# Optimization experiments

Measured on AMD Instinct MI355X. Metric: run time of the kernel, lower is better.

Reference implementation:

```python
import jax, jax.numpy as jnp
import numpy as np

LAYER_NUM = 2
NUM_CLS = 128
HIDDEN = 256
NUM_NODES = 1024


def setup_inputs() -> dict:
    key = jax.random.key(0)
    ks = jax.random.split(key, 12)
    s = 0.05
    return {
        "x": jax.random.normal(ks[0], (NUM_NODES, HIDDEN), jnp.float32),
        "knowledge": jax.random.uniform(ks[1], (NUM_CLS, NUM_CLS), jnp.float32) / NUM_CLS,
        "w3w": jax.random.normal(ks[2], (HIDDEN, 2 * HIDDEN), jnp.float32) * s,
        "b3w": jax.random.normal(ks[3], (HIDDEN,), jnp.float32) * s,
        "u3": jax.random.normal(ks[4], (HIDDEN, HIDDEN), jnp.float32) * s,
        "bu3": jax.random.normal(ks[5], (HIDDEN,), jnp.float32) * s,
        "w4w": jax.random.normal(ks[6], (HIDDEN, 2 * HIDDEN), jnp.float32) * s,
        "b4w": jax.random.normal(ks[7], (HIDDEN,), jnp.float32) * s,
        "w5w": jax.random.normal(ks[8], (HIDDEN, 2 * HIDDEN), jnp.float32) * s,
        "b5w": jax.random.normal(ks[9], (HIDDEN,), jnp.float32) * s,
        "u5": jax.random.normal(ks[10], (HIDDEN, HIDDEN), jnp.float32) * s,
        "bu5": jax.random.normal(ks[11], (HIDDEN,), jnp.float32) * s,
    }


def reference(x, knowledge, w3w, b3w, u3, bu3, w4w, b4w, w5w, b5w, u5, bu5):
    N, H = x.shape
    C = knowledge.shape[0]
    # hidden[n, c, :] = x[n, :]  (repeat per class)
    hidden = jnp.broadcast_to(x[:, None, :], (N, C, H))
    for _ in range(LAYER_NUM):
        hs = hidden.sum(0)                      # [C, H]
        diff = hs[None, :, :] - hidden          # [N, C, H]
        # knowledge.T @ diff_n  and  knowledge @ diff_n, vectorized over nodes
        left = jnp.einsum('kc,nkh->nch', knowledge, diff)
        right = jnp.einsum('ck,nkh->nch', knowledge, diff)
        av = jnp.concatenate([left, right], axis=-1).reshape(N * C, 2 * H)
        h = hidden.reshape(N * C, H)
        uh3 = h @ u3.T + bu3                    # shared: rv uses fc_eq3_u (source quirk)
        zv = jax.nn.sigmoid(av @ w3w.T + b3w + uh3)
        rv = jax.nn.sigmoid(av @ w4w.T + b4w + uh3)
        hv = jnp.tanh(av @ w5w.T + b5w + (rv * h) @ u5.T + bu5)
        h = (1.0 - zv) * h + zv * hv
        hidden = h.reshape(N, C, H)
    return hidden
```

## Files before the change

### kernel.cpp

```cpp
#include <hip/hip_runtime.h>
#include <cstdint>
#include <cstddef>


#define NODES 1024
#define NCLS  128
#define HID   256

using frag  = __attribute__((ext_vector_type(8))) short;
using frag4 = __attribute__((ext_vector_type(4))) short;
using f32x4 = __attribute__((ext_vector_type(4))) float;

__device__ __forceinline__ float bf2f(unsigned short h){
  unsigned int u = ((unsigned int)h) << 16;
  float f; __builtin_memcpy(&f, &u, 4); return f;
}
__device__ __forceinline__ unsigned short f2bf(float f){
  unsigned int u; __builtin_memcpy(&u, &f, 4);
  u = (u + 0x7fffu + ((u >> 16) & 1u)) >> 16;
  return (unsigned short)u;
}
__device__ __forceinline__ float sigm(float x){ return 1.0f/(1.0f + __expf(-x)); }
__device__ __forceinline__ float tanh_fast(float x){ return 1.0f - 2.0f/(__expf(2.0f*x) + 1.0f); }

#define GLOBAL_AS(p) ((const __attribute__((address_space(1))) void*)(p))
#define LDS_AS(p)    ((__attribute__((address_space(3))) void*)(p))
#define MFMA16 __builtin_amdgcn_mfma_f32_16x16x32_bf16

template<int OUT_BF16>
__global__ __launch_bounds__(256) void gemm_bf16(
    const unsigned short* __restrict__ A0, int ldA0, int K0,
    const unsigned short* __restrict__ A1, int ldA1,
    const unsigned short* __restrict__ BT, int ldB, long bStride,
    void* __restrict__ Cptr, int ldC,
    int Ntiles, int Ktot, unsigned int aMask, int Mtiles)
{
  __shared__ unsigned short As[4096];
  __shared__ unsigned short Bs[4096];
  const int t   = threadIdx.x;
  const int bid = blockIdx.x;
  const int xcd = bid & 7, slot = bid >> 3;
  const int mtPerX = (Mtiles >= 8) ? (Mtiles >> 3) : 1;
  const int mt = xcd * mtPerX + slot / Ntiles;
  const int nt = slot % Ntiles;
  const int lane = t & 63, w = t >> 6;
  const int wm = w >> 1, wn = w & 1;
  const int r = lane & 15, q = lane >> 4;
  const int m0 = mt * 128, n0 = nt * 128;
  const unsigned short* Bbase = BT + (size_t)mt * (size_t)bStride;

  f32x4 acc[4][4] = {};

  for (int kb = 0; kb < Ktot; kb += 32) {
#pragma unroll
    for (int i = 0; i < 2; ++i) {
      int u  = i * 256 + t;
      int mi = u >> 2;
      int kc = (u & 3) * 8;
      int k  = kb + kc;
      const unsigned short* ga;
      if (k < K0) ga = A0 + (size_t)((unsigned int)(m0 + mi) & aMask) * (size_t)ldA0 + k;
      else        ga = A1 + (size_t)(m0 + mi) * (size_t)ldA1 + (k - K0);
      __builtin_amdgcn_global_load_lds(GLOBAL_AS(ga), LDS_AS(&As[u * 8]), 16, 0, 0);
      const unsigned short* gb = Bbase + (size_t)(n0 + mi) * (size_t)ldB + k;
      __builtin_amdgcn_global_load_lds(GLOBAL_AS(gb), LDS_AS(&Bs[u * 8]), 16, 0, 0);
    }
    __syncthreads();

    frag af[4], bf_[4];
#pragma unroll
    for (int x = 0; x < 4; ++x) {
      af[x]  = *(const frag*)&As[(wm * 64 + x * 16 + r) * 32 + q * 8];
      bf_[x] = *(const frag*)&Bs[(wn * 64 + x * 16 + r) * 32 + q * 8];
    }
#pragma unroll
    for (int x = 0; x < 4; ++x)
#pragma unroll
      for (int y = 0; y < 4; ++y)
        acc[x][y] = MFMA16(af[x], bf_[y], acc[x][y], 0, 0, 0);
    __syncthreads();
  }

#pragma unroll
  for (int x = 0; x < 4; ++x) {
#pragma unroll
    for (int y = 0; y < 4; ++y) {
      int col = n0 + wn * 64 + y * 16 + r;
#pragma unroll
      for (int g = 0; g < 4; ++g) {
        long row = m0 + wm * 64 + x * 16 + q * 4 + g;
        if (OUT_BF16) ((unsigned short*)Cptr)[row * (long)ldC + col] = f2bf(acc[x][y][g]);
        else          ((float*)Cptr)[row * (long)ldC + col] = acc[x][y][g];
      }
    }
  }
}

__global__ __launch_bounds__(512, 2) void gemm_pre(
    const unsigned short* __restrict__ AVH, const unsigned short* __restrict__ H1,
    const unsigned short* __restrict__ WB, unsigned short* __restrict__ PRE)
{
  __shared__ __align__(16) unsigned short SM[65536];
  const int t   = threadIdx.x;
  const int bid = blockIdx.x;
  const int xcd = bid & 7, slot = bid >> 3;
  const int mt = xcd * 64 + slot / 3;
  const int ct = slot % 3;
  const int lane = t & 63, w = t >> 6;
  const int wm = w >> 2, wn = w & 3;
  const int r = lane & 15, q = lane >> 4;
  const int m0 = mt * 256;
  const unsigned short* Wrow = WB + (size_t)(ct * 256) * 768;
  const int nkt = (ct < 2) ? 12 : 8;

  unsigned short* const Ab0 = SM;
  unsigned short* const Ab1 = SM + 16384;
  unsigned short* const Bb0 = SM + 32768;
  unsigned short* const Bb1 = SM + 49152;

  f32x4 acc[8][4] = {};

  const int smi = t >> 3, sc = t & 7;

  auto ISSUE_A = [&](unsigned short* dst, int kt, int rbase) {
    int row = rbase + smi;
    int gc = sc ^ (row & 7);
    const unsigned short* ga;
    if (kt < 8) ga = AVH + (size_t)(m0 + row) * 512 + kt * 64 + gc * 8;
    else        ga = H1  + (size_t)(m0 + row) * 256 + (kt - 8) * 64 + gc * 8;
    __builtin_amdgcn_global_load_lds(GLOBAL_AS(ga), LDS_AS(&dst[row * 64 + sc * 8]), 16, 0, 0);
  };
  auto ISSUE_B = [&](unsigned short* dst, int kt, int rbase) {
    int row = rbase + smi;
    int gc = sc ^ (row & 7);
    __builtin_amdgcn_global_load_lds(GLOBAL_AS(Wrow + (size_t)row * 768 + kt * 64 + gc * 8),
                                     LDS_AS(&dst[row * 64 + sc * 8]), 16, 0, 0);
  };

  ISSUE_B(Bb0, 0, 0); ISSUE_B(Bb0, 0, 64); ISSUE_B(Bb0, 0, 128); ISSUE_B(Bb0, 0, 192);
  ISSUE_A(Ab0, 0, 0); ISSUE_A(Ab0, 0, 128); ISSUE_A(Ab0, 0, 64); ISSUE_A(Ab0, 0, 192);
  asm volatile("s_waitcnt vmcnt(2)" ::: "memory");
  __builtin_amdgcn_s_barrier();

#define PRE_PHASE(XG0, ISSUES, TAIL)                                         \
    {                                                                        \
      int ra0 = wm * 128 + (XG0) * 16 + r, ra1 = ra0 + 16;                   \
      frag a00 = *(const frag*)&A[ra0 * 64 + ((q ^ (ra0 & 7)) * 8)];         \
      frag a01 = *(const frag*)&A[ra0 * 64 + (((4 + q) ^ (ra0 & 7)) * 8)];   \
      frag a10 = *(const frag*)&A[ra1 * 64 + ((q ^ (ra1 & 7)) * 8)];         \
      frag a11 = *(const frag*)&A[ra1 * 64 + (((4 + q) ^ (ra1 & 7)) * 8)];   \
      ISSUES;                                                                \
      __builtin_amdgcn_s_setprio(1);                                         \
      _Pragma("unroll")                                                      \
      for (int y = 0; y < 4; ++y) {                                          \
        acc[(XG0)][y]     = MFMA16(a00, bf[y][0], acc[(XG0)][y], 0, 0, 0);   \
        acc[(XG0)][y]     = MFMA16(a01, bf[y][1], acc[(XG0)][y], 0, 0, 0);   \
        acc[(XG0)+1][y]   = MFMA16(a10, bf[y][0], acc[(XG0)+1][y], 0, 0, 0); \
        acc[(XG0)+1][y]   = MFMA16(a11, bf[y][1], acc[(XG0)+1][y], 0, 0, 0); \
      }                                                                      \
      __builtin_amdgcn_s_setprio(0);                                         \
      TAIL;                                                                  \
      asm volatile("" ::: "memory");                                         \
      __builtin_amdgcn_s_barrier();                                          \
    }

  for (int kt = 0; kt < nkt; ++kt) {
    unsigned short* A  = (kt & 1) ? Ab1 : Ab0;
    unsigned short* B  = (kt & 1) ? Bb1 : Bb0;
    unsigned short* An = (kt & 1) ? Ab0 : Ab1;
    unsigned short* Bn = (kt & 1) ? Bb0 : Bb1;
    const bool more = (kt + 1 < nkt);

    frag bf[4][2];
#pragma unroll
    for (int y = 0; y < 4; ++y) {
      int rb = wn * 64 + y * 16 + r;
      bf[y][0] = *(const frag*)&B[rb * 64 + ((q ^ (rb & 7)) * 8)];
      bf[y][1] = *(const frag*)&B[rb * 64 + (((4 + q) ^ (rb & 7)) * 8)];
    }

    PRE_PHASE(0,
      { if (more) { ISSUE_B(Bn, kt + 1, 0); ISSUE_B(Bn, kt + 1, 64); } },
      { })
    PRE_PHASE(2,
      { if (more) { ISSUE_B(Bn, kt + 1, 128); ISSUE_B(Bn, kt + 1, 192); } },
      { if (more) asm volatile("s_waitcnt vmcnt(4)" ::: "memory");
        else      asm volatile("s_waitcnt vmcnt(0)" ::: "memory"); })
    PRE_PHASE(4,
      { if (more) { ISSUE_A(An, kt + 1, 0); ISSUE_A(An, kt + 1, 128); } },
      { })
    PRE_PHASE(6,
      { if (more) { ISSUE_A(An, kt + 1, 64); ISSUE_A(An, kt + 1, 192); } },
      { if (more) asm volatile("s_waitcnt vmcnt(2)" ::: "memory"); })
  }
#undef PRE_PHASE

  unsigned short* L = SM;
#pragma unroll
  for (int xg = 0; xg < 8; ++xg) {
#pragma unroll
    for (int y = 0; y < 4; ++y) {
      int j = wn * 64 + y * 16 + r;
      int jc = j >> 3, jl = j & 7;
#pragma unroll
      for (int g = 0; g < 4; ++g) {
        int c = wm * 128 + xg * 16 + q * 4 + g;
        L[c * 256 + ((jc ^ (c & 31)) * 8) + jl] = f2bf(acc[xg][y][g]);
      }
    }
  }
  __syncthreads();
#pragma unroll
  for (int rr = 0; rr < 16; ++rr) {
    int unit = rr * 512 + t;
    int row = unit >> 5, ch = unit & 31;
    frag v = *(const frag*)&L[row * 256 + ((ch ^ (row & 31)) * 8)];
    *(frag*)&PRE[(size_t)(m0 + row) * 768 + ct * 256 + ch * 8] = v;
  }
}

__global__ __launch_bounds__(256, 2) void gemm_l1(
    const float* __restrict__ XW, const float* __restrict__ SW,
    const float* __restrict__ x,
    const float* __restrict__ b3, const float* __restrict__ b4,
    const float* __restrict__ b5, const float* __restrict__ bu3,
    const float* __restrict__ bu5,
    const float* __restrict__ colsum, const float* __restrict__ rowsum,
    const unsigned short* __restrict__ u5b,
    const unsigned short* __restrict__ KTbN, const unsigned short* __restrict__ KbN,
    unsigned short* __restrict__ H1, unsigned short* __restrict__ AVH)
{
  __shared__ unsigned short SM[17408];
  unsigned short* As = SM;
  unsigned short* Bs = SM + 4096;
  unsigned short* L  = SM;
  __shared__ float tP1[256], tP2[256], tP3[256], tX[256];
  __shared__ float tZ1[256], tZ2[256], tZ3[256];
  __shared__ float tV1[256], tV2[256], tV3[256];
  __shared__ float tCS[128], tRS[128];

  const int t = threadIdx.x, bid = blockIdx.x;
  const int xcd = bid & 7, slot = bid >> 3;
  const int n  = xcd * 128 + (slot >> 1);
  const int nt = slot & 1;
  const int lane = t & 63, w = t >> 6, wm = w >> 1, wn = w & 1;
  const int r = lane & 15, q = lane >> 4;
  const int n0 = nt * 128;
  const float* xw = XW + (size_t)n * 1792;

  {
    int i = t;
    float xwi0 = xw[i], xwi1 = xw[256 + i], xwi2 = xw[512 + i], xwi3 = xw[768 + i];
    float xwi4 = xw[1024 + i], xwi5 = xw[1280 + i], xwu = xw[1536 + i];
    tP1[i] = SW[512 + i] - xwi2;
    tP2[i] = SW[768 + i] - xwi3;
    tP3[i] = xwu + b4[i] + bu3[i];
    tX[i]  = x[(size_t)n * HID + i];
    tZ1[i] = SW[i] - xwi0;
    tZ2[i] = SW[256 + i] - xwi1;
    tZ3[i] = xwu + b3[i] + bu3[i];
    tV1[i] = SW[1024 + i] - xwi4;
    tV2[i] = SW[1280 + i] - xwi5;
    tV3[i] = b5[i] + bu5[i];
    if (t < 128) { tCS[t] = colsum[t]; tRS[t] = rowsum[t]; }
  }
  __syncthreads();

  f32x4 acc[4][4] = {};

  for (int kb = 0; kb < 256; kb += 32) {
#pragma unroll
    for (int i = 0; i < 2; ++i) {
      int u  = i * 256 + t;
      int mi = u >> 2;
      int c  = u & 3;
      int k  = kb + c * 8;
      int gc = c ^ ((mi >> 1) & 3);
      __builtin_amdgcn_global_load_lds(GLOBAL_AS(u5b + (size_t)(n0 + mi) * 256 + kb + gc * 8),
                                       LDS_AS(&Bs[u * 8]), 16, 0, 0);
      float cs = tCS[mi], rs = tRS[mi];
      frag a;
#pragma unroll
      for (int e = 0; e < 8; ++e) {
        int i2 = k + e;
        float pre = cs * tP1[i2] + rs * tP2[i2] + tP3[i2];
        a[e] = (short)f2bf(sigm(pre) * tX[i2]);
      }
      *(frag*)&As[mi * 32 + (gc * 8)] = a;
    }
    __syncthreads();

    frag af[4], bf_[4];
#pragma unroll
    for (int xx = 0; xx < 4; ++xx) {
      int ra = wm * 64 + xx * 16 + r;
      int rb = wn * 64 + xx * 16 + r;
      af[xx]  = *(const frag*)&As[ra * 32 + ((q ^ ((ra >> 1) & 3)) * 8)];
      bf_[xx] = *(const frag*)&Bs[rb * 32 + ((q ^ ((rb >> 1) & 3)) * 8)];
    }
#pragma unroll
    for (int xx = 0; xx < 4; ++xx)
#pragma unroll
      for (int y = 0; y < 4; ++y)
        acc[xx][y] = MFMA16(af[xx], bf_[y], acc[xx][y], 0, 0, 0);
    __syncthreads();
  }

#pragma unroll
  for (int xx = 0; xx < 4; ++xx) {
#pragma unroll
    for (int y = 0; y < 4; ++y) {
      int j = wn * 64 + y * 16 + r;
      int i = n0 + j;
      frag4 pack;
#pragma unroll
      for (int g = 0; g < 4; ++g) {
        int c = wm * 64 + xx * 16 + q * 4 + g;
        float cs = tCS[c], rs = tRS[c];
        float z  = sigm(cs * tZ1[i] + rs * tZ2[i] + tZ3[i]);
        float p5 = cs * tV1[i] + rs * tV2[i] + tV3[i] + acc[xx][y][g];
        float h1 = (1.0f - z) * tX[i] + z * tanh_fast(p5);
        unsigned short hb = f2bf(h1);
        pack[g] = (short)hb;
        H1[(size_t)(n * 128 + c) * HID + i] = hb;
      }
      *(frag4*)&L[j * 136 + (wm * 64 + xx * 16 + q * 4)] = pack;
    }
  }
  __syncthreads();

#pragma unroll 1
  for (int s = 0; s < 2; ++s) {
    const unsigned short* Ks = s ? KbN : KTbN;
#pragma unroll
    for (int xx = 0; xx < 4; ++xx)
#pragma unroll
      for (int y = 0; y < 4; ++y)
        acc[xx][y] = (f32x4){0.0f, 0.0f, 0.0f, 0.0f};
#pragma unroll
    for (int kb = 0; kb < 4; ++kb) {
      frag af[4], bf_[4];
#pragma unroll
      for (int xx = 0; xx < 4; ++xx) {
        int cp = wm * 64 + xx * 16 + r;
        af[xx] = *(const frag*)(Ks + (size_t)cp * 128 + kb * 32 + q * 8);
        int j = wn * 64 + xx * 16 + r;
        bf_[xx] = *(const frag*)&L[j * 136 + kb * 32 + q * 8];
      }
#pragma unroll
      for (int xx = 0; xx < 4; ++xx)
#pragma unroll
        for (int y = 0; y < 4; ++y)
          acc[xx][y] = MFMA16(af[xx], bf_[y], acc[xx][y], 0, 0, 0);
    }
#pragma unroll
    for (int xx = 0; xx < 4; ++xx)
#pragma unroll
      for (int y = 0; y < 4; ++y) {
        int col = s * 256 + n0 + wn * 64 + y * 16 + r;
#pragma unroll
        for (int g = 0; g < 4; ++g) {
          int cp = wm * 64 + xx * 16 + q * 4 + g;
          AVH[(size_t)(n * 128 + cp) * 512 + col] = f2bf(acc[xx][y][g]);
        }
      }
  }
}

__global__ __launch_bounds__(256) void gemm_l2(
    const unsigned short* __restrict__ PRE, const float* __restrict__ SG,
    const unsigned short* __restrict__ H1, const unsigned short* __restrict__ u5b,
    float* __restrict__ out)
{
  __shared__ unsigned short As[4096], Bs[4096];
  const int t = threadIdx.x, bid = blockIdx.x;
  const int xcd = bid & 7, slot = bid >> 3;
  const int mt = xcd * 128 + (slot >> 1);
  const int nt = slot & 1;
  const int lane = t & 63, w = t >> 6, wm = w >> 1, wn = w & 1;
  const int r = lane & 15, q = lane >> 4;
  const int m0 = mt * 128, n0 = nt * 128;

  f32x4 acc[4][4] = {};

  for (int kb = 0; kb < 256; kb += 32) {
#pragma unroll
    for (int i = 0; i < 2; ++i) {
      int u  = i * 256 + t;
      int mi = u >> 2;
      int c  = u & 3;
      int k  = kb + c * 8;
      int gc = c ^ ((mi >> 1) & 3);
      __builtin_amdgcn_global_load_lds(GLOBAL_AS(u5b + (size_t)(n0 + mi) * 256 + kb + gc * 8),
                                       LDS_AS(&Bs[u * 8]), 16, 0, 0);
      long row = m0 + mi;
      frag p4 = *(const frag*)(PRE + row * 768 + 256 + k);
      frag h1 = *(const frag*)(H1 + row * 256 + k);
      const float* sg = SG + (size_t)mi * 768 + 256 + k;
      frag a;
#pragma unroll
      for (int e = 0; e < 8; ++e) {
        float rv = sigm(sg[e] + bf2f((unsigned short)p4[e]));
        a[e] = (short)f2bf(rv * bf2f((unsigned short)h1[e]));
      }
      *(frag*)&As[mi * 32 + (gc * 8)] = a;
    }
    __syncthreads();

    frag af[4], bf_[4];
#pragma unroll
    for (int xx = 0; xx < 4; ++xx) {
      int ra = wm * 64 + xx * 16 + r;
      int rb = wn * 64 + xx * 16 + r;
      af[xx]  = *(const frag*)&As[ra * 32 + ((q ^ ((ra >> 1) & 3)) * 8)];
      bf_[xx] = *(const frag*)&Bs[rb * 32 + ((q ^ ((rb >> 1) & 3)) * 8)];
    }
#pragma unroll
    for (int xx = 0; xx < 4; ++xx)
#pragma unroll
      for (int y = 0; y < 4; ++y)
        acc[xx][y] = MFMA16(af[xx], bf_[y], acc[xx][y], 0, 0, 0);
    __syncthreads();
  }

#pragma unroll
  for (int xx = 0; xx < 4; ++xx) {
#pragma unroll
    for (int y = 0; y < 4; ++y) {
      int i = n0 + wn * 64 + y * 16 + r;
#pragma unroll
      for (int g = 0; g < 4; ++g) {
        int c = wm * 64 + xx * 16 + q * 4 + g;
        long row = m0 + c;
        float z  = sigm(SG[(size_t)c * 768 + i] + bf2f(PRE[row * 768 + i]));
        float pv = SG[(size_t)c * 768 + 512 + i] + bf2f(PRE[row * 768 + 512 + i])
                 + acc[xx][y][g];
        float h  = bf2f(H1[row * 256 + i]);
        out[row * 256 + i] = (1.0f - z) * h + z * tanh_fast(pv);
      }
    }
  }
}

__global__ __launch_bounds__(256) void prep_cast(
    const float* __restrict__ x, const float* __restrict__ Kn,
    const float* __restrict__ w3, const float* __restrict__ u3,
    const float* __restrict__ w4, const float* __restrict__ w5,
    const float* __restrict__ u5,
    unsigned short* __restrict__ xb, unsigned short* __restrict__ WB,
    unsigned short* __restrict__ WB2, unsigned short* __restrict__ u5b,
    unsigned short* __restrict__ KbN, unsigned short* __restrict__ KTbN)
{
  int idx = blockIdx.x * 256 + threadIdx.x;
  if (idx < 262144) { xb[idx] = f2bf(x[idx]); return; }
  idx -= 262144;
  if (idx < 589824) {
    int col = idx / 768, j = idx % 768;
    int g = col >> 8, i = col & 255;
    float v;
    if (j < 512) { const float* wg = (g == 0) ? w3 : (g == 1) ? w4 : w5; v = wg[(size_t)i * 512 + j]; }
    else v = (g < 2) ? u3[(size_t)i * 256 + (j - 512)] : 0.0f;
    WB[(size_t)col * 768 + j] = f2bf(v);
    return;
  }
  idx -= 589824;
  if (idx < 458752) {
    int col = idx / 256, h = idx % 256;
    int b = col >> 8, i = col & 255;
    float v = (b < 6) ? ((b < 2 ? w3 : (b < 4 ? w4 : w5))[(size_t)i * 512 + (b & 1) * 256 + h])
                      : u3[(size_t)i * 256 + h];
    WB2[(size_t)col * 256 + h] = f2bf(v);
    return;
  }
  idx -= 458752;
  if (idx < 65536) { u5b[idx] = f2bf(u5[idx]); return; }
  idx -= 65536;
  if (idx < 16384) { int c = idx >> 7, k = idx & 127; KbN[idx]  = f2bf(-Kn[c * 128 + k]); return; }
  idx -= 16384;
  { int c = idx >> 7, k = idx & 127; KTbN[idx] = f2bf(-Kn[k * 128 + c]); }
}

__global__ __launch_bounds__(256) void prep_reduce(
    const float* __restrict__ x, const float* __restrict__ Kn,
    float* __restrict__ S, float* __restrict__ colsum, float* __restrict__ rowsum)
{
  int b = blockIdx.x, t = threadIdx.x;
  if (b < 8) {
    float s = 0.f;
    for (int n = 0; n < 128; ++n) s += x[(size_t)(b * 128 + n) * HID + t];
    atomicAdd(&S[t], s);
  } else if (b == 8) {
    if (t < NCLS) { float s = 0.f; for (int k = 0; k < NCLS; ++k) s += Kn[k * NCLS + t]; colsum[t] = s; }
  } else {
    if (t < NCLS) { float s = 0.f; for (int k = 0; k < NCLS; ++k) s += Kn[t * NCLS + k]; rowsum[t] = s; }
  }
}

__global__ __launch_bounds__(256) void prep_sw(
    const float* __restrict__ S, const float* __restrict__ w3,
    const float* __restrict__ w4, const float* __restrict__ w5, float* __restrict__ SW)
{
  int col = blockIdx.x * 256 + threadIdx.x;
  int b = col >> 8, i = col & 255;
  const float* w = (b < 2) ? w3 : (b < 4) ? w4 : w5;
  const float* row = w + (size_t)i * 512 + (b & 1) * 256;
  float s = 0.f;
  for (int h = 0; h < HID; ++h) s += S[h] * row[h];
  SW[col] = s;
}

__global__ __launch_bounds__(256) void reduce_hs(
    const unsigned short* __restrict__ H1, float* __restrict__ hs)
{
  int bid = blockIdx.x;
  int c = bid >> 5, nch = bid & 31;
  int i = threadIdx.x;
  const unsigned short* p = H1 + (size_t)nch * 32 * NCLS * HID + (size_t)c * HID + i;
  float s = 0.f;
  for (int n = 0; n < 32; ++n) s += bf2f(p[(size_t)n * NCLS * HID]);
  atomicAdd(&hs[c * HID + i], s);
}

__global__ __launch_bounds__(256) void p2a(
    const float* __restrict__ hs, const float* __restrict__ w3,
    const float* __restrict__ w4, const float* __restrict__ w5, float* __restrict__ hsW)
{
  __shared__ float hrow[HID];
  int k = blockIdx.x & 127, b = blockIdx.x >> 7;
  int t = threadIdx.x;
  hrow[t] = hs[k * HID + t];
  __syncthreads();
  const float* w = (b < 2) ? w3 : (b < 4) ? w4 : w5;
  const float* row = w + (size_t)t * 512 + (b & 1) * 256;
  float s = 0.f;
  for (int h = 0; h < HID; ++h) s += hrow[h] * row[h];
  hsW[(size_t)k * 1536 + b * 256 + t] = s;
}

__global__ __launch_bounds__(256) void p2b(
    const float* __restrict__ hsW, const float* __restrict__ Kn,
    const float* __restrict__ b3, const float* __restrict__ b4, const float* __restrict__ b5,
    const float* __restrict__ bu3, const float* __restrict__ bu5, float* __restrict__ SG)
{
  __shared__ float kc[NCLS], kr[NCLS];
  int c = blockIdx.x, t = threadIdx.x;
  if (t < NCLS) { kc[t] = Kn[t * NCLS + c]; kr[t] = Kn[c * NCLS + t]; }
  __syncthreads();
  for (int g = 0; g < 3; ++g) {
    int i = t;
    const float* L = hsW + (size_t)(2 * g) * 256 + i;
    const float* R = hsW + (size_t)(2 * g + 1) * 256 + i;
    float s = 0.f;
    for (int k = 0; k < NCLS; ++k) s += kc[k] * L[(size_t)k * 1536] + kr[k] * R[(size_t)k * 1536];
    const float* bg = (g == 0) ? b3 : (g == 1) ? b4 : b5;
    s += bg[i] + ((g < 2) ? bu3[i] : bu5[i]);
    SG[(size_t)c * 768 + g * 256 + i] = s;
  }
}

extern "C" void kernel_launch(void* const* d_in, const int* in_sizes, int n_in,
                              void* d_out, int out_size, void* d_ws, size_t ws_size,
                              hipStream_t stream) {
  (void)in_sizes; (void)n_in; (void)out_size; (void)ws_size;
  const float* x   = (const float*)d_in[0];
  const float* Kn  = (const float*)d_in[1];
  const float* w3  = (const float*)d_in[2];
  const float* b3  = (const float*)d_in[3];
  const float* u3  = (const float*)d_in[4];
  const float* bu3 = (const float*)d_in[5];
  const float* w4  = (const float*)d_in[6];
  const float* b4  = (const float*)d_in[7];
  const float* w5  = (const float*)d_in[8];
  const float* b5  = (const float*)d_in[9];
  const float* u5  = (const float*)d_in[10];
  const float* bu5 = (const float*)d_in[11];
  float* out = (float*)d_out;

  char* w = (char*)d_ws;
  unsigned short* AVH = (unsigned short*)(w);
  unsigned short* PRE = (unsigned short*)(w + 134217728);
  unsigned short* H1  = (unsigned short*)(w + 335544320);
  float*          XW  = (float*)(w + 402653184);
  char* misc = w + 409993216;
  float* S      = (float*)(misc);
  float* hs     = (float*)(misc + 1024);
  float* SW     = (float*)(misc + 132096);
  float* colsum = (float*)(misc + 138240);
  float* rowsum = (float*)(misc + 138752);
  float* hsW    = (float*)(misc + 139264);
  float* SG     = (float*)(misc + 925696);
  unsigned short* WB   = (unsigned short*)(misc + 1318912);
  unsigned short* WB2  = (unsigned short*)(misc + 2498560);
  unsigned short* u5b  = (unsigned short*)(misc + 3416064);
  unsigned short* KbN  = (unsigned short*)(misc + 3547136);
  unsigned short* KTbN = (unsigned short*)(misc + 3579904);
  unsigned short* xb   = (unsigned short*)(misc + 3612672);

  hipMemsetAsync(misc, 0, 132096, stream);

  prep_cast<<<5504, 256, 0, stream>>>(x, Kn, w3, u3, w4, w5, u5, xb, WB, WB2, u5b, KbN, KTbN);
  prep_reduce<<<10, 256, 0, stream>>>(x, Kn, S, colsum, rowsum);
  prep_sw<<<6, 256, 0, stream>>>(S, w3, w4, w5, SW);

  gemm_bf16<0><<<8 * 14, 256, 0, stream>>>(xb, 256, 256, xb, 256, WB2, 256, 0L,
                                           (void*)XW, 1792, 14, 256, 0xFFFFFFFFu, 8);
  gemm_l1<<<2048, 256, 0, stream>>>(XW, SW, x, b3, b4, b5, bu3, bu5,
                                    colsum, rowsum, u5b, KTbN, KbN, H1, AVH);

  reduce_hs<<<4096, 256, 0, stream>>>(H1, hs);
  p2a<<<768, 256, 0, stream>>>(hs, w3, w4, w5, hsW);
  p2b<<<128, 256, 0, stream>>>(hsW, Kn, b3, b4, b5, bu3, bu5, SG);

  gemm_pre<<<1536, 512, 0, stream>>>(AVH, H1, WB, PRE);

  gemm_l2<<<2048, 256, 0, stream>>>(PRE, SG, H1, u5b, out);
}
```

Before: 699.4 us.

## Fuse reset-gate product into gemm_pre epilogue and retile gemm_l2 with pipelined LDS

gemm_pre now computes sigmoid(rv)*h for the rv columns in its epilogue and writes that product into PRE. gemm_l2 therefore reads a ready bf16 A operand through direct global-to-LDS loads instead of recomputing the gate while staging. gemm_l2 is also rewritten to use 256x256 tiles, 512 threads, K-tile 64 and double-buffered async loads with prefetch interleaved into the MFMA phases. Its epilogue goes through an LDS transpose so the final GRU update is done with vectorized coalesced stores. The cost is more LDS use per block and fewer, larger blocks (512), which may lower occupancy or leave the tail unbalanced.

```diff
diff --git a/kernel.cpp b/kernel.cpp
--- a/kernel.cpp
+++ b/kernel.cpp
@@ -98,7 +98,8 @@
 
 __global__ __launch_bounds__(512, 2) void gemm_pre(
     const unsigned short* __restrict__ AVH, const unsigned short* __restrict__ H1,
-    const unsigned short* __restrict__ WB, unsigned short* __restrict__ PRE)
+    const unsigned short* __restrict__ WB, const float* __restrict__ SG,
+    unsigned short* __restrict__ PRE)
 {
   __shared__ __align__(16) unsigned short SM[65536];
   const int t   = threadIdx.x;
@@ -210,12 +211,34 @@
     }
   }
   __syncthreads();
-#pragma unroll
-  for (int rr = 0; rr < 16; ++rr) {
-    int unit = rr * 512 + t;
-    int row = unit >> 5, ch = unit & 31;
-    frag v = *(const frag*)&L[row * 256 + ((ch ^ (row & 31)) * 8)];
-    *(frag*)&PRE[(size_t)(m0 + row) * 768 + ct * 256 + ch * 8] = v;
+  if (ct == 1) {
+#pragma unroll
+    for (int rr = 0; rr < 16; ++rr) {
+      int unit = rr * 512 + t;
+      int row = unit >> 5, ch = unit & 31;
+      size_t grow = (size_t)(m0 + row);
+      frag v  = *(const frag*)&L[row * 256 + ((ch ^ (row & 31)) * 8)];
+      frag hh = *(const frag*)(H1 + grow * 256 + ch * 8);
+      const float* sgr = SG + (size_t)(row & 127) * 768 + 256 + ch * 8;
+      f32x4 s0 = *(const f32x4*)(sgr);
+      f32x4 s1 = *(const f32x4*)(sgr + 4);
+      frag o;
+#pragma unroll
+      for (int e = 0; e < 8; ++e) {
+        float sv = (e < 4) ? s0[e] : s1[e - 4];
+        float rv = sigm(sv + bf2f((unsigned short)v[e]));
+        o[e] = (short)f2bf(rv * bf2f((unsigned short)hh[e]));
+      }
+      *(frag*)&PRE[grow * 768 + 256 + ch * 8] = o;
+    }
+  } else {
+#pragma unroll
+    for (int rr = 0; rr < 16; ++rr) {
+      int unit = rr * 512 + t;
+      int row = unit >> 5, ch = unit & 31;
+      frag v = *(const frag*)&L[row * 256 + ((ch ^ (row & 31)) * 8)];
+      *(frag*)&PRE[(size_t)(m0 + row) * 768 + ct * 256 + ch * 8] = v;
+    }
   }
 }
 
@@ -367,77 +390,152 @@
   }
 }
 
-__global__ __launch_bounds__(256) void gemm_l2(
+__global__ __launch_bounds__(512, 2) void gemm_l2(
     const unsigned short* __restrict__ PRE, const float* __restrict__ SG,
     const unsigned short* __restrict__ H1, const unsigned short* __restrict__ u5b,
     float* __restrict__ out)
 {
-  __shared__ unsigned short As[4096], Bs[4096];
+  __shared__ __align__(16) unsigned short SM[65536];
   const int t = threadIdx.x, bid = blockIdx.x;
   const int xcd = bid & 7, slot = bid >> 3;
-  const int mt = xcd * 128 + (slot >> 1);
-  const int nt = slot & 1;
-  const int lane = t & 63, w = t >> 6, wm = w >> 1, wn = w & 1;
+  const int mt = xcd * 64 + slot;
+  const int lane = t & 63, w = t >> 6;
+  const int wm = w >> 2, wn = w & 3;
   const int r = lane & 15, q = lane >> 4;
-  const int m0 = mt * 128, n0 = nt * 128;
-
-  f32x4 acc[4][4] = {};
-
-  for (int kb = 0; kb < 256; kb += 32) {
-#pragma unroll
-    for (int i = 0; i < 2; ++i) {
-      int u  = i * 256 + t;
-      int mi = u >> 2;
-      int c  = u & 3;
-      int k  = kb + c * 8;
-      int gc = c ^ ((mi >> 1) & 3);
-      __builtin_amdgcn_global_load_lds(GLOBAL_AS(u5b + (size_t)(n0 + mi) * 256 + kb + gc * 8),
-                                       LDS_AS(&Bs[u * 8]), 16, 0, 0);
-      long row = m0 + mi;
-      frag p4 = *(const frag*)(PRE + row * 768 + 256 + k);
-      frag h1 = *(const frag*)(H1 + row * 256 + k);
-      const float* sg = SG + (size_t)mi * 768 + 256 + k;
-      frag a;
+  const int m0 = mt * 256;
+  const int nkt = 4;
+
+  unsigned short* const Ab0 = SM;
+  unsigned short* const Ab1 = SM + 16384;
+  unsigned short* const Bb0 = SM + 32768;
+  unsigned short* const Bb1 = SM + 49152;
+
+  f32x4 acc[8][4] = {};
+
+  const int smi = t >> 3, sc = t & 7;
+
+  auto ISSUE_A = [&](unsigned short* dst, int kt, int rbase) {
+    int row = rbase + smi;
+    int gc = sc ^ (row & 7);
+    const unsigned short* ga = PRE + (size_t)(m0 + row) * 768 + 256 + kt * 64 + gc * 8;
+    __builtin_amdgcn_global_load_lds(GLOBAL_AS(ga), LDS_AS(&dst[row * 64 + sc * 8]), 16, 0, 0);
+  };
+  auto ISSUE_B = [&](unsigned short* dst, int kt, int rbase) {
+    int row = rbase + smi;
+    int gc = sc ^ (row & 7);
+    __builtin_amdgcn_global_load_lds(GLOBAL_AS(u5b + (size_t)row * 256 + kt * 64 + gc * 8),
+                                     LDS_AS(&dst[row * 64 + sc * 8]), 16, 0, 0);
+  };
+
+  ISSUE_B(Bb0, 0, 0); ISSUE_B(Bb0, 0, 64); ISSUE_B(Bb0, 0, 128); ISSUE_B(Bb0, 0, 192);
+  ISSUE_A(Ab0, 0, 0); ISSUE_A(Ab0, 0, 128); ISSUE_A(Ab0, 0, 64); ISSUE_A(Ab0, 0, 192);
+  asm volatile("s_waitcnt vmcnt(2)" ::: "memory");
+  __builtin_amdgcn_s_barrier();
+
+#define L2_PHASE(XG0, ISSUES, TAIL)                                          \
+    {                                                                        \
+      int ra0 = wm * 128 + (XG0) * 16 + r, ra1 = ra0 + 16;                   \
+      frag a00 = *(const frag*)&A[ra0 * 64 + ((q ^ (ra0 & 7)) * 8)];         \
+      frag a01 = *(const frag*)&A[ra0 * 64 + (((4 + q) ^ (ra0 & 7)) * 8)];   \
+      frag a10 = *(const frag*)&A[ra1 * 64 + ((q ^ (ra1 & 7)) * 8)];         \
+      frag a11 = *(const frag*)&A[ra1 * 64 + (((4 + q) ^ (ra1 & 7)) * 8)];   \
+      ISSUES;                                                                \
+      __builtin_amdgcn_s_setprio(1);                                         \
+      _Pragma("unroll")                                                      \
+      for (int y = 0; y < 4; ++y) {                                          \
+        acc[(XG0)][y]     = MFMA16(a00, bf[y][0], acc[(XG0)][y], 0, 0, 0);   \
+        acc[(XG0)][y]     = MFMA16(a01, bf[y][1], acc[(XG0)][y], 0, 0, 0);   \
+        acc[(XG0)+1][y]   = MFMA16(a10, bf[y][0], acc[(XG0)+1][y], 0, 0, 0); \
+        acc[(XG0)+1][y]   = MFMA16(a11, bf[y][1], acc[(XG0)+1][y], 0, 0, 0); \
+      }                                                                      \
+      __builtin_amdgcn_s_setprio(0);                                         \
+      TAIL;                                                                  \
+      asm volatile("" ::: "memory");                                         \
+      __builtin_amdgcn_s_barrier();                                          \
+    }
+
+  for (int kt = 0; kt < nkt; ++kt) {
+    unsigned short* A  = (kt & 1) ? Ab1 : Ab0;
+    unsigned short* B  = (kt & 1) ? Bb1 : Bb0;
+    unsigned short* An = (kt & 1) ? Ab0 : Ab1;
+    unsigned short* Bn = (kt & 1) ? Bb0 : Bb1;
+    const bool more = (kt + 1 < nkt);
+
+    frag bf[4][2];
+#pragma unroll
+    for (int y = 0; y < 4; ++y) {
+      int rb = wn * 64 + y * 16 + r;
+      bf[y][0] = *(const frag*)&B[rb * 64 + ((q ^ (rb & 7)) * 8)];
+      bf[y][1] = *(const frag*)&B[rb * 64 + (((4 + q) ^ (rb & 7)) * 8)];
+    }
+
+    L2_PHASE(0,
+      { if (more) { ISSUE_B(Bn, kt + 1, 0); ISSUE_B(Bn, kt + 1, 64); } },
+      { })
+    L2_PHASE(2,
+      { if (more) { ISSUE_B(Bn, kt + 1, 128); ISSUE_B(Bn, kt + 1, 192); } },
+      { if (more) asm volatile("s_waitcnt vmcnt(4)" ::: "memory");
+        else      asm volatile("s_waitcnt vmcnt(0)" ::: "memory"); })
+    L2_PHASE(4,
+      { if (more) { ISSUE_A(An, kt + 1, 0); ISSUE_A(An, kt + 1, 128); } },
+      { })
+    L2_PHASE(6,
+      { if (more) { ISSUE_A(An, kt + 1, 64); ISSUE_A(An, kt + 1, 192); } },
+      { if (more) asm volatile("s_waitcnt vmcnt(2)" ::: "memory"); })
+  }
+#undef L2_PHASE
+
+  float* L = (float*)SM;
+#pragma unroll 1
+  for (int p = 0; p < 2; ++p) {
+    if (p) __syncthreads();
+    if (wm == p) {
+#pragma unroll
+      for (int xg = 0; xg < 8; ++xg)
+#pragma unroll
+        for (int y = 0; y < 4; ++y) {
+          int j = wn * 64 + y * 16 + r;
+#pragma unroll
+          for (int g = 0; g < 4; ++g) {
+            int lr = xg * 16 + q * 4 + g;
+            L[lr * 256 + (j ^ ((lr & 7) << 2))] = acc[xg][y][g];
+          }
+        }
+    }
+    __syncthreads();
+#pragma unroll
+    for (int rr = 0; rr < 8; ++rr) {
+      int unit = rr * 512 + t;
+      int row = unit >> 5, ch = unit & 31;
+      size_t grow = (size_t)(m0 + p * 128 + row);
+      int c = (int)(grow & 127);
+      int j0 = ch * 8;
+      const int off = (row & 7) << 2;
+      f32x4 a0 = *(const f32x4*)&L[row * 256 + (j0 ^ off)];
+      f32x4 a1 = *(const f32x4*)&L[row * 256 + ((j0 + 4) ^ off)];
+      const unsigned short* prow = PRE + grow * 768;
+      frag pz = *(const frag*)(prow + j0);
+      frag pp = *(const frag*)(prow + 512 + j0);
+      frag hh = *(const frag*)(H1 + grow * 256 + j0);
+      const float* sgr = SG + (size_t)c * 768;
+      f32x4 sz0 = *(const f32x4*)(sgr + j0);
+      f32x4 sz1 = *(const f32x4*)(sgr + j0 + 4);
+      f32x4 sp0 = *(const f32x4*)(sgr + 512 + j0);
+      f32x4 sp1 = *(const f32x4*)(sgr + 512 + j0 + 4);
+      f32x4 o0, o1;
 #pragma unroll
       for (int e = 0; e < 8; ++e) {
-        float rv = sigm(sg[e] + bf2f((unsigned short)p4[e]));
-        a[e] = (short)f2bf(rv * bf2f((unsigned short)h1[e]));
+        float sz = (e < 4) ? sz0[e] : sz1[e - 4];
+        float sp = (e < 4) ? sp0[e] : sp1[e - 4];
+        float av = (e < 4) ? a0[e] : a1[e - 4];
+        float z  = sigm(sz + bf2f((unsigned short)pz[e]));
+        float pv = sp + bf2f((unsigned short)pp[e]) + av;
+        float h  = bf2f((unsigned short)hh[e]);
+        float o  = (1.0f - z) * h + z * tanh_fast(pv);
+        if (e < 4) o0[e] = o; else o1[e - 4] = o;
       }
-      *(frag*)&As[mi * 32 + (gc * 8)] = a;
-    }
-    __syncthreads();
-
-    frag af[4], bf_[4];
-#pragma unroll
-    for (int xx = 0; xx < 4; ++xx) {
-      int ra = wm * 64 + xx * 16 + r;
-      int rb = wn * 64 + xx * 16 + r;
-      af[xx]  = *(const frag*)&As[ra * 32 + ((q ^ ((ra >> 1) & 3)) * 8)];
-      bf_[xx] = *(const frag*)&Bs[rb * 32 + ((q ^ ((rb >> 1) & 3)) * 8)];
-    }
-#pragma unroll
-    for (int xx = 0; xx < 4; ++xx)
-#pragma unroll
-      for (int y = 0; y < 4; ++y)
-        acc[xx][y] = MFMA16(af[xx], bf_[y], acc[xx][y], 0, 0, 0);
-    __syncthreads();
-  }
-
-#pragma unroll
-  for (int xx = 0; xx < 4; ++xx) {
-#pragma unroll
-    for (int y = 0; y < 4; ++y) {
-      int i = n0 + wn * 64 + y * 16 + r;
-#pragma unroll
-      for (int g = 0; g < 4; ++g) {
-        int c = wm * 64 + xx * 16 + q * 4 + g;
-        long row = m0 + c;
-        float z  = sigm(SG[(size_t)c * 768 + i] + bf2f(PRE[row * 768 + i]));
-        float pv = SG[(size_t)c * 768 + 512 + i] + bf2f(PRE[row * 768 + 512 + i])
-                 + acc[xx][y][g];
-        float h  = bf2f(H1[row * 256 + i]);
-        out[row * 256 + i] = (1.0f - z) * h + z * tanh_fast(pv);
-      }
+      *(f32x4*)&out[grow * 256 + j0] = o0;
+      *(f32x4*)&out[grow * 256 + j0 + 4] = o1;
     }
   }
 }
@@ -611,7 +709,7 @@
   p2a<<<768, 256, 0, stream>>>(hs, w3, w4, w5, hsW);
   p2b<<<128, 256, 0, stream>>>(hsW, Kn, b3, b4, b5, bu3, bu5, SG);
 
-  gemm_pre<<<1536, 512, 0, stream>>>(AVH, H1, WB, PRE);
-
-  gemm_l2<<<2048, 256, 0, stream>>>(PRE, SG, H1, u5b, out);
-}
+  gemm_pre<<<1536, 512, 0, stream>>>(AVH, H1, WB, SG, PRE);
+
+  gemm_l2<<<512, 512, 0, stream>>>(PRE, SG, H1, u5b, out);
+}
```

After: 842.7 us. +20.5%, slower.
